# Optimization experiments

Hardware: AMD Instinct MI355X
Metric: run time of the kernel (lower is better)

## Reference

```python
import jax, jax.numpy as jnp
import numpy as np

THRESH = 0.01  # confidence threshold on max softmax prob

def setup_inputs() -> dict:
    key = jax.random.key(0)
    ks = jax.random.split(key, 14)
    B, D, H, C = 8192, 2048, 2048, 1000
    sD = 1.0 / np.sqrt(D)
    sH = 1.0 / np.sqrt(H)
    return {
        "x":   jax.random.normal(ks[0], (B, D), jnp.float32),
        "W1":  jax.random.normal(ks[1], (D, H), jnp.float32) * sD,
        "b1":  jnp.zeros((H,), jnp.float32),
        "W2":  jax.random.normal(ks[2], (H, H), jnp.float32) * sH,
        "b2":  jnp.zeros((H,), jnp.float32),
        "W3":  jax.random.normal(ks[3], (H, H), jnp.float32) * sH,
        "b3":  jnp.zeros((H,), jnp.float32),
        "H1w": jax.random.normal(ks[4], (H, C), jnp.float32) * sH,
        "H1b": jnp.zeros((C,), jnp.float32),
        "H2w": jax.random.normal(ks[5], (H, C), jnp.float32) * sH,
        "H2b": jnp.zeros((C,), jnp.float32),
        "Fw":  jax.random.normal(ks[6], (H, C), jnp.float32) * sH,
        "Fb":  jnp.zeros((C,), jnp.float32),
    }

def _confident(logits):
    # confidence_function: max softmax probability exceeds threshold
    p = jax.nn.softmax(logits, axis=-1)
    return jnp.max(p, axis=-1) > THRESH  # [B] bool

def reference(x, W1, b1, W2, b2, W3, b3, H1w, H1b, H2w, H2b, Fw, Fb):
    # Stage 1 backbone + partial head
    h1 = jax.nn.relu(x @ W1 + b1)          # [B,H]
    p1 = h1 @ H1w + H1b                     # [B,C]
    c1 = _confident(p1)                     # exit mask stage 1
    # Stage 2 backbone + partial head
    h2 = jax.nn.relu(h1 @ W2 + b2)
    p2 = h2 @ H2w + H2b
    c2 = _confident(p2)
    # Final stage
    h3 = jax.nn.relu(h2 @ W3 + b3)
    p3 = h3 @ Fw + Fb
    # Per-sample first-exit selection == original index_select/index_copy cascade
    out = jnp.where(c1[:, None], p1, jnp.where(c2[:, None], p2, p3))
    return out
```

## Files before the change

kernel.cpp:

```cpp
#include <hip/hip_runtime.h>
#include <math.h>

typedef __bf16 bf16x8 __attribute__((ext_vector_type(8)));
typedef float f32x4 __attribute__((ext_vector_type(4)));
typedef unsigned short ushort_t;
typedef unsigned int uint_t;

__device__ __forceinline__ ushort_t f2bf(float f) {
    uint_t u = __float_as_uint(f);
    u += 0x7fff + ((u >> 16) & 1);
    return (ushort_t)(u >> 16);
}
__device__ __forceinline__ float bf2f(ushort_t h) {
    return __uint_as_float(((uint_t)h) << 16);
}

__device__ __forceinline__ size_t poff(int row, int k, int Kdim) {
    return ((((size_t)(row >> 7) * (Kdim >> 5) + (k >> 5)) * 512)
            + ((k >> 3) & 3) * 128 + (row & 127)) * 8 + (k & 7);
}

__device__ __forceinline__ void ll16(const ushort_t* g, ushort_t* l) {
    __builtin_amdgcn_global_load_lds(
        (const __attribute__((address_space(1))) unsigned int*)g,
        (__attribute__((address_space(3))) unsigned int*)l, 16, 0, 0);
}

template <int N> __device__ __forceinline__ void wait_vmcnt() {
    if constexpr (N == 0) asm volatile("s_waitcnt vmcnt(0)" ::: "memory");
    else if constexpr (N == 1) asm volatile("s_waitcnt vmcnt(1)" ::: "memory");
    else if constexpr (N == 2) asm volatile("s_waitcnt vmcnt(2)" ::: "memory");
    else if constexpr (N == 3) asm volatile("s_waitcnt vmcnt(3)" ::: "memory");
    else if constexpr (N == 4) asm volatile("s_waitcnt vmcnt(4)" ::: "memory");
    else if constexpr (N == 5) asm volatile("s_waitcnt vmcnt(5)" ::: "memory");
    else asm volatile("s_waitcnt vmcnt(6)" ::: "memory");
}
__device__ __forceinline__ void lgkm0_fence() {
    asm volatile("s_waitcnt lgkmcnt(0)" ::: "memory");
    __builtin_amdgcn_sched_barrier(0);
}

__global__ __launch_bounds__(256) void split_kernel(
    const float* __restrict__ in, ushort_t* __restrict__ hi,
    ushort_t* __restrict__ lo, int Kdim)
{
    const int i = blockIdx.x * 256 + threadIdx.x;
    const int row = i >> 8;
    const int k = (i & 255) * 8;
    const float4 v0 = *(const float4*)(in + (size_t)row * Kdim + k);
    const float4 v1 = *(const float4*)(in + (size_t)row * Kdim + k + 4);
    const float f[8] = {v0.x, v0.y, v0.z, v0.w, v1.x, v1.y, v1.z, v1.w};
    ushort_t h[8], l[8];
    #pragma unroll
    for (int j = 0; j < 8; ++j) {
        h[j] = f2bf(f[j]);
        l[j] = f2bf(f[j] - bf2f(h[j]));
    }
    const size_t o = poff(row, k, Kdim);
    *(uint4*)(hi + o) = *(const uint4*)h;
    *(uint4*)(lo + o) = *(const uint4*)l;
}

__global__ __launch_bounds__(256) void tsplit_kernel(
    const float* __restrict__ W, ushort_t* __restrict__ hi,
    ushort_t* __restrict__ lo, int K, int N, int write_lo)
{
    __shared__ float t[32][33];
    const int tx = threadIdx.x & 31;
    const int ty = threadIdx.x >> 5;
    const int nb = blockIdx.x * 32;
    const int kb = blockIdx.y * 32;
    #pragma unroll
    for (int i = 0; i < 4; ++i) {
        int k = kb + ty + i * 8;
        int n = nb + tx;
        t[ty + i * 8][tx] = (n < N) ? W[(size_t)k * N + n] : 0.f;
    }
    __syncthreads();
    #pragma unroll
    for (int i = 0; i < 4; ++i) {
        int n = nb + ty + i * 8;
        int k = kb + tx;
        float f = t[tx][ty + i * 8];
        size_t idx = poff(n, k, K);
        ushort_t h = f2bf(f);
        hi[idx] = h;
        if (write_lo) lo[idx] = f2bf(f - bf2f(h));
    }
}

__global__ __launch_bounds__(256) void gather_pack(
    const ushort_t* __restrict__ srchi, const ushort_t* __restrict__ srclo,
    ushort_t* __restrict__ dsthi, ushort_t* __restrict__ dstlo,
    const int* __restrict__ idx, const int* __restrict__ cntp, int Kdim)
{
    const int j = blockIdx.x;
    if (j >= *cntp) return;
    const int srow = idx[j];
    const int k = threadIdx.x * 8;
    const size_t so = poff(srow, k, Kdim);
    const size_t dofs = poff(j, k, Kdim);
    *(uint4*)(dsthi + dofs) = *(const uint4*)(srchi + so);
    if (srclo) *(uint4*)(dstlo + dofs) = *(const uint4*)(srclo + so);
}


template <int BN>
__global__ __launch_bounds__(512, 2) void gemm_split3(
    const ushort_t* __restrict__ Ahi, const ushort_t* __restrict__ Alo,
    const ushort_t* __restrict__ Bhi, const ushort_t* __restrict__ Blo,
    const float* __restrict__ bias,
    float* __restrict__ Cf, ushort_t* __restrict__ Chi, ushort_t* __restrict__ Clo,
    int K, int Ntrue, int ldc, int relu_flag,
    const int* __restrict__ cntp, int Mfull)
{
    static_assert(BN == 256 || BN == 128, "BN");
    constexpr int BSLAB = BN / 128;
    constexpr int NF = BN / 64;
    constexpr int SH = 2 + BSLAB;
    constexpr int T = 2 * SH;

    __shared__ __align__(16) ushort_t sAh[2][8192];
    __shared__ __align__(16) ushort_t sAl[2][8192];
    __shared__ __align__(16) ushort_t sBh[2][BSLAB * 4096];
    __shared__ __align__(16) ushort_t sBl[2][BSLAB * 4096];

    const int tid = threadIdx.x;
    const int m0 = blockIdx.y * 256;
    const int n0 = blockIdx.x * BN;
    int Meff = Mfull;
    if (cntp) Meff = *cntp;
    if (m0 >= ((Meff + 255) & ~255)) return;

    const int lane = tid & 63, wave = tid >> 6;
    const int wm = wave >> 2, wn = wave & 3;
    const int q = lane >> 4, r16 = lane & 15;
    const int wofs = wave * 512;

    const size_t bstr = (size_t)(K >> 5) * 4096;
    const ushort_t* gAh = Ahi + (size_t)(2 * blockIdx.y) * bstr + tid * 8;
    const ushort_t* gAl = Alo + (size_t)(2 * blockIdx.y) * bstr + tid * 8;
    const ushort_t* gBh = Bhi + (size_t)(BSLAB * blockIdx.x) * bstr + tid * 8;
    const ushort_t* gBl = Blo + (size_t)(BSLAB * blockIdx.x) * bstr + tid * 8;

    int aoff[8], boff[NF];
    #pragma unroll
    for (int mi = 0; mi < 8; ++mi)
        aoff[mi] = wm * 4096 + (q * 128 + mi * 16 + r16) * 8;
    #pragma unroll
    for (int nj = 0; nj < NF; ++nj) {
        const int col = wn * (NF * 16) + nj * 16 + r16;
        boff[nj] = (col >> 7) * 4096 + (q * 128 + (col & 127)) * 8;
    }

    f32x4 acc[8][NF];
    #pragma unroll
    for (int mi = 0; mi < 8; ++mi)
        #pragma unroll
        for (int nj = 0; nj < NF; ++nj) acc[mi][nj] = (f32x4)(0.f);

    const int NT = K >> 5;

    ll16(gAh, &sAh[0][wofs]);
    ll16(gAh + bstr, &sAh[0][4096 + wofs]);
    ll16(gBh, &sBh[0][wofs]);
    if constexpr (BSLAB == 2) ll16(gBh + bstr, &sBh[0][4096 + wofs]);
    ll16(gBl, &sBl[0][wofs]);
    if constexpr (BSLAB == 2) ll16(gBl + bstr, &sBl[0][4096 + wofs]);
    ll16(gAl, &sAl[0][wofs]);
    ll16(gAl + bstr, &sAl[0][4096 + wofs]);

    bf16x8 ah[8], bh[NF];
    for (int t = 0; t < NT - 1; ++t) {
        const int c = t & 1;
        const size_t ko = (size_t)(t + 1) * 4096;

        wait_vmcnt<T - SH>();
        __builtin_amdgcn_s_barrier();
        #pragma unroll
        for (int mi = 0; mi < 8; ++mi) ah[mi] = *(const bf16x8*)(&sAh[c][aoff[mi]]);
        #pragma unroll
        for (int nj = 0; nj < NF; ++nj) bh[nj] = *(const bf16x8*)(&sBh[c][boff[nj]]);
        ll16(gAh + ko, &sAh[c ^ 1][wofs]);
        ll16(gAh + bstr + ko, &sAh[c ^ 1][4096 + wofs]);
        ll16(gBh + ko, &sBh[c ^ 1][wofs]);
        if constexpr (BSLAB == 2) ll16(gBh + bstr + ko, &sBh[c ^ 1][4096 + wofs]);
        lgkm0_fence();
        __builtin_amdgcn_s_setprio(1);
        #pragma unroll
        for (int nj = 0; nj < NF; ++nj)
            #pragma unroll
            for (int mi = 0; mi < 8; ++mi)
                acc[mi][nj] = __builtin_amdgcn_mfma_f32_16x16x32_bf16(ah[mi], bh[nj], acc[mi][nj], 0, 0, 0);
        __builtin_amdgcn_s_setprio(0);

        wait_vmcnt<T - BSLAB>();
        __builtin_amdgcn_s_barrier();
        bf16x8 bl[NF];
        #pragma unroll
        for (int nj = 0; nj < NF; ++nj) bl[nj] = *(const bf16x8*)(&sBl[c][boff[nj]]);
        ll16(gBl + ko, &sBl[c ^ 1][wofs]);
        if constexpr (BSLAB == 2) ll16(gBl + bstr + ko, &sBl[c ^ 1][4096 + wofs]);
        lgkm0_fence();
        __builtin_amdgcn_s_setprio(1);
        #pragma unroll
        for (int nj = 0; nj < NF; ++nj)
            #pragma unroll
            for (int mi = 0; mi < 8; ++mi)
                acc[mi][nj] = __builtin_amdgcn_mfma_f32_16x16x32_bf16(ah[mi], bl[nj], acc[mi][nj], 0, 0, 0);
        __builtin_amdgcn_s_setprio(0);

        wait_vmcnt<T - 2>();
        __builtin_amdgcn_s_barrier();
        bf16x8 al[8];
        #pragma unroll
        for (int mi = 0; mi < 8; ++mi) al[mi] = *(const bf16x8*)(&sAl[c][aoff[mi]]);
        ll16(gAl + ko, &sAl[c ^ 1][wofs]);
        ll16(gAl + bstr + ko, &sAl[c ^ 1][4096 + wofs]);
        lgkm0_fence();
        __builtin_amdgcn_s_setprio(1);
        #pragma unroll
        for (int nj = 0; nj < NF; ++nj)
            #pragma unroll
            for (int mi = 0; mi < 8; ++mi)
                acc[mi][nj] = __builtin_amdgcn_mfma_f32_16x16x32_bf16(al[mi], bh[nj], acc[mi][nj], 0, 0, 0);
        __builtin_amdgcn_s_setprio(0);
    }

    {
        const int c = (NT - 1) & 1;
        wait_vmcnt<T - SH>();
        __builtin_amdgcn_s_barrier();
        #pragma unroll
        for (int mi = 0; mi < 8; ++mi) ah[mi] = *(const bf16x8*)(&sAh[c][aoff[mi]]);
        #pragma unroll
        for (int nj = 0; nj < NF; ++nj) bh[nj] = *(const bf16x8*)(&sBh[c][boff[nj]]);
        lgkm0_fence();
        __builtin_amdgcn_s_setprio(1);
        #pragma unroll
        for (int nj = 0; nj < NF; ++nj)
            #pragma unroll
            for (int mi = 0; mi < 8; ++mi)
                acc[mi][nj] = __builtin_amdgcn_mfma_f32_16x16x32_bf16(ah[mi], bh[nj], acc[mi][nj], 0, 0, 0);
        __builtin_amdgcn_s_setprio(0);

        wait_vmcnt<2>();
        __builtin_amdgcn_s_barrier();
        bf16x8 bl[NF];
        #pragma unroll
        for (int nj = 0; nj < NF; ++nj) bl[nj] = *(const bf16x8*)(&sBl[c][boff[nj]]);
        lgkm0_fence();
        __builtin_amdgcn_s_setprio(1);
        #pragma unroll
        for (int nj = 0; nj < NF; ++nj)
            #pragma unroll
            for (int mi = 0; mi < 8; ++mi)
                acc[mi][nj] = __builtin_amdgcn_mfma_f32_16x16x32_bf16(ah[mi], bl[nj], acc[mi][nj], 0, 0, 0);
        __builtin_amdgcn_s_setprio(0);

        wait_vmcnt<0>();
        __builtin_amdgcn_s_barrier();
        bf16x8 al[8];
        #pragma unroll
        for (int mi = 0; mi < 8; ++mi) al[mi] = *(const bf16x8*)(&sAl[c][aoff[mi]]);
        lgkm0_fence();
        __builtin_amdgcn_s_setprio(1);
        #pragma unroll
        for (int nj = 0; nj < NF; ++nj)
            #pragma unroll
            for (int mi = 0; mi < 8; ++mi)
                acc[mi][nj] = __builtin_amdgcn_mfma_f32_16x16x32_bf16(al[mi], bh[nj], acc[mi][nj], 0, 0, 0);
        __builtin_amdgcn_s_setprio(0);
    }

    #pragma unroll
    for (int mi = 0; mi < 8; ++mi) {
        #pragma unroll
        for (int nj = 0; nj < NF; ++nj) {
            const int col = n0 + wn * (NF * 16) + nj * 16 + r16;
            const int rowb = m0 + wm * 128 + mi * 16 + q * 4;
            const float bv = (col < Ntrue) ? bias[col] : 0.f;
            #pragma unroll
            for (int r = 0; r < 4; ++r) {
                float v = acc[mi][nj][r] + bv;
                if (relu_flag) v = fmaxf(v, 0.f);
                if (Cf) {
                    if (col < Ntrue) Cf[(size_t)(rowb + r) * ldc + col] = v;
                } else {
                    const size_t idx = poff(rowb + r, col, ldc);
                    ushort_t h = f2bf(v);
                    Chi[idx] = h;
                    Clo[idx] = f2bf(v - bf2f(h));
                }
            }
        }
    }
}

template <int BN>
__global__ __launch_bounds__(512, 2) void gemm_bf16k(
    const ushort_t* __restrict__ Ahi, const ushort_t* __restrict__ Bhi,
    const float* __restrict__ bias,
    float* __restrict__ Cf, ushort_t* __restrict__ Chi,
    int K, int Ntrue, int ldc, int relu_flag,
    const int* __restrict__ cntp, int Mfull)
{
    static_assert(BN == 256 || BN == 128, "BN");
    constexpr int BSLAB = BN / 128;
    constexpr int NF = BN / 64;
    constexpr int SH = 2 + BSLAB;

    __shared__ __align__(16) ushort_t sA[4][8192];
    __shared__ __align__(16) ushort_t sB[4][BSLAB * 4096];

    const int tid = threadIdx.x;
    const int m0 = blockIdx.y * 256;
    const int n0 = blockIdx.x * BN;
    int Meff = Mfull;
    if (cntp) Meff = *cntp;
    if (m0 >= ((Meff + 255) & ~255)) return;

    const int lane = tid & 63, wave = tid >> 6;
    const int wm = wave >> 2, wn = wave & 3;
    const int q = lane >> 4, r16 = lane & 15;
    const int wofs = wave * 512;

    const size_t bstr = (size_t)(K >> 5) * 4096;
    const ushort_t* gA = Ahi + (size_t)(2 * blockIdx.y) * bstr + tid * 8;
    const ushort_t* gB = Bhi + (size_t)(BSLAB * blockIdx.x) * bstr + tid * 8;

    int aoff[8], boff[NF];
    #pragma unroll
    for (int mi = 0; mi < 8; ++mi)
        aoff[mi] = wm * 4096 + (q * 128 + mi * 16 + r16) * 8;
    #pragma unroll
    for (int nj = 0; nj < NF; ++nj) {
        const int col = wn * (NF * 16) + nj * 16 + r16;
        boff[nj] = (col >> 7) * 4096 + (q * 128 + (col & 127)) * 8;
    }

    f32x4 acc[8][NF];
    #pragma unroll
    for (int mi = 0; mi < 8; ++mi)
        #pragma unroll
        for (int nj = 0; nj < NF; ++nj) acc[mi][nj] = (f32x4)(0.f);

    const int NT = K >> 5;

    #pragma unroll
    for (int tt = 0; tt < 2; ++tt) {
        const size_t ko = (size_t)tt * 4096;
        ll16(gA + ko, &sA[tt][wofs]);
        ll16(gA + bstr + ko, &sA[tt][4096 + wofs]);
        ll16(gB + ko, &sB[tt][wofs]);
        if constexpr (BSLAB == 2) ll16(gB + bstr + ko, &sB[tt][4096 + wofs]);
    }

    bf16x8 ah[8], bh[NF];
    for (int t = 0; t < NT - 1; ++t) {
        const int c = t & 3;
        wait_vmcnt<SH>();
        __builtin_amdgcn_s_barrier();
        #pragma unroll
        for (int mi = 0; mi < 8; ++mi) ah[mi] = *(const bf16x8*)(&sA[c][aoff[mi]]);
        #pragma unroll
        for (int nj = 0; nj < NF; ++nj) bh[nj] = *(const bf16x8*)(&sB[c][boff[nj]]);
        if (t + 2 < NT) {
            const int c2 = (t + 2) & 3;
            const size_t ko = (size_t)(t + 2) * 4096;
            ll16(gA + ko, &sA[c2][wofs]);
            ll16(gA + bstr + ko, &sA[c2][4096 + wofs]);
            ll16(gB + ko, &sB[c2][wofs]);
            if constexpr (BSLAB == 2) ll16(gB + bstr + ko, &sB[c2][4096 + wofs]);
        }
        lgkm0_fence();
        __builtin_amdgcn_s_setprio(1);
        #pragma unroll
        for (int nj = 0; nj < NF; ++nj)
            #pragma unroll
            for (int mi = 0; mi < 8; ++mi)
                acc[mi][nj] = __builtin_amdgcn_mfma_f32_16x16x32_bf16(ah[mi], bh[nj], acc[mi][nj], 0, 0, 0);
        __builtin_amdgcn_s_setprio(0);
    }
    {
        const int c = (NT - 1) & 3;
        wait_vmcnt<0>();
        __builtin_amdgcn_s_barrier();
        #pragma unroll
        for (int mi = 0; mi < 8; ++mi) ah[mi] = *(const bf16x8*)(&sA[c][aoff[mi]]);
        #pragma unroll
        for (int nj = 0; nj < NF; ++nj) bh[nj] = *(const bf16x8*)(&sB[c][boff[nj]]);
        lgkm0_fence();
        __builtin_amdgcn_s_setprio(1);
        #pragma unroll
        for (int nj = 0; nj < NF; ++nj)
            #pragma unroll
            for (int mi = 0; mi < 8; ++mi)
                acc[mi][nj] = __builtin_amdgcn_mfma_f32_16x16x32_bf16(ah[mi], bh[nj], acc[mi][nj], 0, 0, 0);
        __builtin_amdgcn_s_setprio(0);
    }

    #pragma unroll
    for (int mi = 0; mi < 8; ++mi) {
        #pragma unroll
        for (int nj = 0; nj < NF; ++nj) {
            const int col = n0 + wn * (NF * 16) + nj * 16 + r16;
            const int rowb = m0 + wm * 128 + mi * 16 + q * 4;
            const float bv = (col < Ntrue) ? bias[col] : 0.f;
            #pragma unroll
            for (int r = 0; r < 4; ++r) {
                float v = acc[mi][nj][r] + bv;
                if (relu_flag) v = fmaxf(v, 0.f);
                if (Cf) {
                    if (col < Ntrue) Cf[(size_t)(rowb + r) * ldc + col] = v;
                } else {
                    const size_t idx = poff(rowb + r, col, ldc);
                    Chi[idx] = f2bf(v);
                }
            }
        }
    }
}

__global__ __launch_bounds__(256) void conf_kernel(
    const float* __restrict__ P, int N, int* __restrict__ cm,
    const int* __restrict__ cntp)
{
    const int b = blockIdx.x;
    if (cntp && b >= *cntp) return;
    const float* row = P + (size_t)b * N;
    float m = -3.0e38f;
    for (int c = threadIdx.x; c < N; c += 256) m = fmaxf(m, row[c]);
    #pragma unroll
    for (int off = 32; off > 0; off >>= 1) m = fmaxf(m, __shfl_down(m, off));
    __shared__ float red_max[4];
    __shared__ float red_sum[4];
    const int wave = threadIdx.x >> 6;
    const int lane = threadIdx.x & 63;
    if (lane == 0) red_max[wave] = m;
    __syncthreads();
    m = fmaxf(fmaxf(red_max[0], red_max[1]), fmaxf(red_max[2], red_max[3]));
    float s = 0.f;
    for (int c = threadIdx.x; c < N; c += 256) s += expf(row[c] - m);
    #pragma unroll
    for (int off = 32; off > 0; off >>= 1) s += __shfl_down(s, off);
    if (lane == 0) red_sum[wave] = s;
    __syncthreads();
    if (threadIdx.x == 0) {
        float tot = red_sum[0] + red_sum[1] + red_sum[2] + red_sum[3];
        cm[b] = (tot < 100.0f) ? 1 : 0;
    }
}

__global__ void init_kernel(int* cnt1, int* cnt2) {
    if (threadIdx.x == 0) { *cnt1 = 0; *cnt2 = 0; }
}

__global__ __launch_bounds__(256) void build_kernel(
    const int* __restrict__ mask, int n, const int* __restrict__ nlimp,
    int* __restrict__ cnt, int* __restrict__ idx)
{
    int i = blockIdx.x * 256 + threadIdx.x;
    int nl = nlimp ? *nlimp : n;
    if (i >= nl) return;
    if (!mask[i]) { int p = atomicAdd(cnt, 1); idx[p] = i; }
}

__global__ __launch_bounds__(256) void scatter2_kernel(
    float* __restrict__ out, const float* __restrict__ p2,
    const int* __restrict__ idx1, const int* __restrict__ c2m,
    const int* __restrict__ cntp, int N)
{
    const int j = blockIdx.y;
    if (j >= *cntp || !c2m[j]) return;
    const int c = blockIdx.x * 256 + threadIdx.x;
    if (c >= N) return;
    out[(size_t)idx1[j] * N + c] = p2[(size_t)j * N + c];
}

__global__ __launch_bounds__(256) void scatter3_kernel(
    float* __restrict__ out, const float* __restrict__ p3,
    const int* __restrict__ idx1, const int* __restrict__ idx2,
    const int* __restrict__ cntp, int N)
{
    const int jj = blockIdx.y;
    if (jj >= *cntp) return;
    const int c = blockIdx.x * 256 + threadIdx.x;
    if (c >= N) return;
    out[(size_t)idx1[idx2[jj]] * N + c] = p3[(size_t)jj * N + c];
}

extern "C" void kernel_launch(void* const* d_in, const int* in_sizes, int n_in,
                              void* d_out, int out_size, void* d_ws, size_t ws_size,
                              hipStream_t stream)
{
    const float* x   = (const float*)d_in[0];
    const float* W1  = (const float*)d_in[1];
    const float* b1  = (const float*)d_in[2];
    const float* W2  = (const float*)d_in[3];
    const float* b2  = (const float*)d_in[4];
    const float* W3  = (const float*)d_in[5];
    const float* b3  = (const float*)d_in[6];
    const float* H1w = (const float*)d_in[7];
    const float* H1b = (const float*)d_in[8];
    const float* H2w = (const float*)d_in[9];
    const float* H2b = (const float*)d_in[10];
    const float* Fw  = (const float*)d_in[11];
    const float* Fb  = (const float*)d_in[12];
    float* out = (float*)d_out;

    const int B = 8192, D = 2048, Hh = 2048, Cc = 1000;

    ushort_t* xhi  = (ushort_t*)d_ws;
    ushort_t* xlo  = xhi + (size_t)B * D;
    ushort_t* h1hi = xlo + (size_t)B * D;
    ushort_t* h1lo = h1hi + (size_t)B * Hh;
    ushort_t* W0hi = h1lo + (size_t)B * Hh;
    ushort_t* W0lo = W0hi + (size_t)Hh * Hh;
    ushort_t* W1thi = W0lo + (size_t)Hh * Hh;
    ushort_t* W1tlo = W1thi + (size_t)1024 * Hh;
    float* p2 = (float*)(W1tlo + (size_t)1024 * Hh);
    int* c1   = (int*)(p2 + (size_t)B * Cc);
    int* c2m  = c1 + B;
    int* idx1 = c2m + B;
    int* idx2 = idx1 + B;
    int* cnt1 = idx2 + B;
    int* cnt2 = cnt1 + 1;

    ushort_t* h1chi = xhi;  ushort_t* h1clo = xlo;
    ushort_t* h2hi = h1hi;  ushort_t* h2lo = h1lo;
    ushort_t* h2chi = xhi;
    ushort_t* h3hi = h1hi;
    float* p3 = (float*)xlo;

    dim3 blk(256);
    dim3 blk5(512);
    const dim3 gBB(Hh / 256, B / 256);
    const dim3 gHD(1024 / 128, B / 256);
    const dim3 gT2(64, 64);
    const dim3 gTH(32, 64);

    init_kernel<<<1, 64, 0, stream>>>(cnt1, cnt2);

    split_kernel<<<dim3(B * D / 8 / 256), blk, 0, stream>>>(x, xhi, xlo, D);
    tsplit_kernel<<<gT2, blk, 0, stream>>>(W1, W0hi, W0lo, D, Hh, 1);
    gemm_split3<256><<<gBB, blk5, 0, stream>>>(xhi, xlo, W0hi, W0lo, b1,
                                               nullptr, h1hi, h1lo, D, Hh, Hh, 1,
                                               nullptr, B);
    tsplit_kernel<<<gTH, blk, 0, stream>>>(H1w, W1thi, W1tlo, Hh, Cc, 1);
    gemm_split3<128><<<gHD, blk5, 0, stream>>>(h1hi, h1lo, W1thi, W1tlo, H1b,
                                               out, nullptr, nullptr, Hh, Cc, Cc, 0,
                                               nullptr, B);
    conf_kernel<<<dim3(B), blk, 0, stream>>>(out, Cc, c1, nullptr);
    build_kernel<<<dim3(B / 256), blk, 0, stream>>>(c1, B, nullptr, cnt1, idx1);

    gather_pack<<<dim3(B), blk, 0, stream>>>(h1hi, h1lo, h1chi, h1clo, idx1, cnt1, Hh);
    tsplit_kernel<<<gT2, blk, 0, stream>>>(W2, W0hi, W0lo, Hh, Hh, 1);
    gemm_split3<256><<<gBB, blk5, 0, stream>>>(h1chi, h1clo, W0hi, W0lo, b2,
                                               nullptr, h2hi, h2lo, Hh, Hh, Hh, 1,
                                               cnt1, B);
    tsplit_kernel<<<gTH, blk, 0, stream>>>(H2w, W1thi, W1tlo, Hh, Cc, 1);
    gemm_split3<128><<<gHD, blk5, 0, stream>>>(h2hi, h2lo, W1thi, W1tlo, H2b,
                                               p2, nullptr, nullptr, Hh, Cc, Cc, 0,
                                               cnt1, B);
    conf_kernel<<<dim3(B), blk, 0, stream>>>(p2, Cc, c2m, cnt1);
    build_kernel<<<dim3(B / 256), blk, 0, stream>>>(c2m, B, cnt1, cnt2, idx2);

    gather_pack<<<dim3(B), blk, 0, stream>>>(h2hi, nullptr, h2chi, nullptr, idx2, cnt2, Hh);
    tsplit_kernel<<<gT2, blk, 0, stream>>>(W3, W0hi, nullptr, Hh, Hh, 0);
    gemm_bf16k<256><<<gBB, blk5, 0, stream>>>(h2chi, W0hi, b3,
                                              nullptr, h3hi, Hh, Hh, Hh, 1,
                                              cnt2, B);
    tsplit_kernel<<<gTH, blk, 0, stream>>>(Fw, W1thi, nullptr, Hh, Cc, 0);
    gemm_bf16k<128><<<gHD, blk5, 0, stream>>>(h3hi, W1thi, Fb,
                                              p3, nullptr, Hh, Cc, Cc, 0,
                                              cnt2, B);

    scatter2_kernel<<<dim3((Cc + 255) / 256, B), blk, 0, stream>>>(out, p2, idx1, c2m, cnt1, Cc);
    scatter3_kernel<<<dim3((Cc + 255) / 256, B), blk, 0, stream>>>(out, p3, idx1, idx2, cnt2, Cc);
}
```

Measured before the change: 1.025 ms.

## Drop LDS wait fences in GEMM loops, fuse index build into confidence kernel

The explicit lgkmcnt(0) waits before each MFMA block are removed and only the scheduling barriers are kept. This leaves the compiler free to place finer-grained waits on the LDS fragment loads so they can overlap with the MFMAs. The separate build_kernel is folded into conf_kernel, which appends non-confident row indices through an atomic counter, saving two launches and a pass over the mask. The scatter kernels now use one block per row with a strided loop instead of a 2D grid, which is meant to cut the number of blocks that exit immediately.

```diff
diff --git a/kernel.cpp b/kernel.cpp
--- a/kernel.cpp
+++ b/kernel.cpp
@@ -35,10 +35,6 @@
     else if constexpr (N == 5) asm volatile("s_waitcnt vmcnt(5)" ::: "memory");
     else asm volatile("s_waitcnt vmcnt(6)" ::: "memory");
 }
-__device__ __forceinline__ void lgkm0_fence() {
-    asm volatile("s_waitcnt lgkmcnt(0)" ::: "memory");
-    __builtin_amdgcn_sched_barrier(0);
-}
 
 __global__ __launch_bounds__(256) void split_kernel(
     const float* __restrict__ in, ushort_t* __restrict__ hi,
@@ -185,7 +181,7 @@
         ll16(gAh + bstr + ko, &sAh[c ^ 1][4096 + wofs]);
         ll16(gBh + ko, &sBh[c ^ 1][wofs]);
         if constexpr (BSLAB == 2) ll16(gBh + bstr + ko, &sBh[c ^ 1][4096 + wofs]);
-        lgkm0_fence();
+        __builtin_amdgcn_sched_barrier(0);
         __builtin_amdgcn_s_setprio(1);
         #pragma unroll
         for (int nj = 0; nj < NF; ++nj)
@@ -201,7 +197,7 @@
         for (int nj = 0; nj < NF; ++nj) bl[nj] = *(const bf16x8*)(&sBl[c][boff[nj]]);
         ll16(gBl + ko, &sBl[c ^ 1][wofs]);
         if constexpr (BSLAB == 2) ll16(gBl + bstr + ko, &sBl[c ^ 1][4096 + wofs]);
-        lgkm0_fence();
+        __builtin_amdgcn_sched_barrier(0);
         __builtin_amdgcn_s_setprio(1);
         #pragma unroll
         for (int nj = 0; nj < NF; ++nj)
@@ -217,7 +213,7 @@
         for (int mi = 0; mi < 8; ++mi) al[mi] = *(const bf16x8*)(&sAl[c][aoff[mi]]);
         ll16(gAl + ko, &sAl[c ^ 1][wofs]);
         ll16(gAl + bstr + ko, &sAl[c ^ 1][4096 + wofs]);
-        lgkm0_fence();
+        __builtin_amdgcn_sched_barrier(0);
         __builtin_amdgcn_s_setprio(1);
         #pragma unroll
         for (int nj = 0; nj < NF; ++nj)
@@ -235,7 +231,6 @@
         for (int mi = 0; mi < 8; ++mi) ah[mi] = *(const bf16x8*)(&sAh[c][aoff[mi]]);
         #pragma unroll
         for (int nj = 0; nj < NF; ++nj) bh[nj] = *(const bf16x8*)(&sBh[c][boff[nj]]);
-        lgkm0_fence();
         __builtin_amdgcn_s_setprio(1);
         #pragma unroll
         for (int nj = 0; nj < NF; ++nj)
@@ -249,7 +244,6 @@
         bf16x8 bl[NF];
         #pragma unroll
         for (int nj = 0; nj < NF; ++nj) bl[nj] = *(const bf16x8*)(&sBl[c][boff[nj]]);
-        lgkm0_fence();
         __builtin_amdgcn_s_setprio(1);
         #pragma unroll
         for (int nj = 0; nj < NF; ++nj)
@@ -263,7 +257,6 @@
         bf16x8 al[8];
         #pragma unroll
         for (int mi = 0; mi < 8; ++mi) al[mi] = *(const bf16x8*)(&sAl[c][aoff[mi]]);
-        lgkm0_fence();
         __builtin_amdgcn_s_setprio(1);
         #pragma unroll
         for (int nj = 0; nj < NF; ++nj)
@@ -373,7 +366,7 @@
             ll16(gB + ko, &sB[c2][wofs]);
             if constexpr (BSLAB == 2) ll16(gB + bstr + ko, &sB[c2][4096 + wofs]);
         }
-        lgkm0_fence();
+        __builtin_amdgcn_sched_barrier(0);
         __builtin_amdgcn_s_setprio(1);
         #pragma unroll
         for (int nj = 0; nj < NF; ++nj)
@@ -390,7 +383,6 @@
         for (int mi = 0; mi < 8; ++mi) ah[mi] = *(const bf16x8*)(&sA[c][aoff[mi]]);
         #pragma unroll
         for (int nj = 0; nj < NF; ++nj) bh[nj] = *(const bf16x8*)(&sB[c][boff[nj]]);
-        lgkm0_fence();
         __builtin_amdgcn_s_setprio(1);
         #pragma unroll
         for (int nj = 0; nj < NF; ++nj)
@@ -424,7 +416,8 @@
 
 __global__ __launch_bounds__(256) void conf_kernel(
     const float* __restrict__ P, int N, int* __restrict__ cm,
-    const int* __restrict__ cntp)
+    const int* __restrict__ cntp, int* __restrict__ cnt_out,
+    int* __restrict__ idx_out)
 {
     const int b = blockIdx.x;
     if (cntp && b >= *cntp) return;
@@ -448,22 +441,14 @@
     __syncthreads();
     if (threadIdx.x == 0) {
         float tot = red_sum[0] + red_sum[1] + red_sum[2] + red_sum[3];
-        cm[b] = (tot < 100.0f) ? 1 : 0;
+        int conf = (tot < 100.0f) ? 1 : 0;
+        if (cm) cm[b] = conf;
+        if (!conf) { int p = atomicAdd(cnt_out, 1); idx_out[p] = b; }
     }
 }
 
 __global__ void init_kernel(int* cnt1, int* cnt2) {
     if (threadIdx.x == 0) { *cnt1 = 0; *cnt2 = 0; }
-}
-
-__global__ __launch_bounds__(256) void build_kernel(
-    const int* __restrict__ mask, int n, const int* __restrict__ nlimp,
-    int* __restrict__ cnt, int* __restrict__ idx)
-{
-    int i = blockIdx.x * 256 + threadIdx.x;
-    int nl = nlimp ? *nlimp : n;
-    if (i >= nl) return;
-    if (!mask[i]) { int p = atomicAdd(cnt, 1); idx[p] = i; }
 }
 
 __global__ __launch_bounds__(256) void scatter2_kernel(
@@ -471,11 +456,11 @@
     const int* __restrict__ idx1, const int* __restrict__ c2m,
     const int* __restrict__ cntp, int N)
 {
-    const int j = blockIdx.y;
+    const int j = blockIdx.x;
     if (j >= *cntp || !c2m[j]) return;
-    const int c = blockIdx.x * 256 + threadIdx.x;
-    if (c >= N) return;
-    out[(size_t)idx1[j] * N + c] = p2[(size_t)j * N + c];
+    float* dst = out + (size_t)idx1[j] * N;
+    const float* src = p2 + (size_t)j * N;
+    for (int c = threadIdx.x; c < N; c += 256) dst[c] = src[c];
 }
 
 __global__ __launch_bounds__(256) void scatter3_kernel(
@@ -483,11 +468,11 @@
     const int* __restrict__ idx1, const int* __restrict__ idx2,
     const int* __restrict__ cntp, int N)
 {
-    const int jj = blockIdx.y;
+    const int jj = blockIdx.x;
     if (jj >= *cntp) return;
-    const int c = blockIdx.x * 256 + threadIdx.x;
-    if (c >= N) return;
-    out[(size_t)idx1[idx2[jj]] * N + c] = p3[(size_t)jj * N + c];
+    float* dst = out + (size_t)idx1[idx2[jj]] * N;
+    const float* src = p3 + (size_t)jj * N;
+    for (int c = threadIdx.x; c < N; c += 256) dst[c] = src[c];
 }
 
 extern "C" void kernel_launch(void* const* d_in, const int* in_sizes, int n_in,
@@ -551,8 +536,7 @@
     gemm_split3<128><<<gHD, blk5, 0, stream>>>(h1hi, h1lo, W1thi, W1tlo, H1b,
                                                out, nullptr, nullptr, Hh, Cc, Cc, 0,
                                                nullptr, B);
-    conf_kernel<<<dim3(B), blk, 0, stream>>>(out, Cc, c1, nullptr);
-    build_kernel<<<dim3(B / 256), blk, 0, stream>>>(c1, B, nullptr, cnt1, idx1);
+    conf_kernel<<<dim3(B), blk, 0, stream>>>(out, Cc, nullptr, nullptr, cnt1, idx1);
 
     gather_pack<<<dim3(B), blk, 0, stream>>>(h1hi, h1lo, h1chi, h1clo, idx1, cnt1, Hh);
     tsplit_kernel<<<gT2, blk, 0, stream>>>(W2, W0hi, W0lo, Hh, Hh, 1);
@@ -563,8 +547,7 @@
     gemm_split3<128><<<gHD, blk5, 0, stream>>>(h2hi, h2lo, W1thi, W1tlo, H2b,
                                                p2, nullptr, nullptr, Hh, Cc, Cc, 0,
                                                cnt1, B);
-    conf_kernel<<<dim3(B), blk, 0, stream>>>(p2, Cc, c2m, cnt1);
-    build_kernel<<<dim3(B / 256), blk, 0, stream>>>(c2m, B, cnt1, cnt2, idx2);
+    conf_kernel<<<dim3(B), blk, 0, stream>>>(p2, Cc, c2m, cnt1, cnt2, idx2);
 
     gather_pack<<<dim3(B), blk, 0, stream>>>(h2hi, nullptr, h2chi, nullptr, idx2, cnt2, Hh);
     tsplit_kernel<<<gT2, blk, 0, stream>>>(W3, W0hi, nullptr, Hh, Hh, 0);
@@ -576,6 +559,6 @@
                                               p3, nullptr, Hh, Cc, Cc, 0,
                                               cnt2, B);
 
-    scatter2_kernel<<<dim3((Cc + 255) / 256, B), blk, 0, stream>>>(out, p2, idx1, c2m, cnt1, Cc);
-    scatter3_kernel<<<dim3((Cc + 255) / 256, B), blk, 0, stream>>>(out, p3, idx1, idx2, cnt2, Cc);
-}
+    scatter2_kernel<<<dim3(B), blk, 0, stream>>>(out, p2, idx1, c2m, cnt1, Cc);
+    scatter3_kernel<<<dim3(B), blk, 0, stream>>>(out, p3, idx1, idx2, cnt2, Cc);
+}
```

Result: slower. 1.143 ms (+11.5%).
